# Optimization experiments

Measured on AMD Instinct MI355X. Metric: run time of the kernel, lower is better.

Reference implementation:

```python
import jax, jax.numpy as jnp
import numpy as np

B = 4            # batch (num sequences)
T = 1024         # tokens per sequence (prefill, context_length == tokens_per_seq)
D_MODEL = 4096
H = 32           # n_heads
KVH = 8          # n_kv_heads
HD = D_MODEL // H          # 128
NREP = H // KVH            # 4
BLOCK = 16                 # kv-cache block size
NBLK_PER_SEQ = T // BLOCK  # 64
NBLK = B * NBLK_PER_SEQ    # 256
LAYER_IDX = 0


def _rope(x, positions, cos, sin):
    # x: [N, h, HD]; cos/sin: [max_pos, HD//2]
    c = cos[positions][:, None, :]
    s = sin[positions][:, None, :]
    x1 = x[..., 0::2]
    x2 = x[..., 1::2]
    out = jnp.stack([x1 * c - x2 * s, x1 * s + x2 * c], axis=-1)
    return out.reshape(x.shape)


def setup_inputs() -> dict:
    key = jax.random.key(0)
    ks = jax.random.split(key, 4)
    N = B * T
    x = jax.random.normal(ks[0], (N, D_MODEL), jnp.float32) * 0.02
    w_q = jax.random.normal(ks[1], (D_MODEL, H * HD), jnp.float32) * 0.02
    w_kv = jax.random.normal(ks[2], (D_MODEL, 2 * KVH * HD), jnp.float32) * 0.02
    w_o = jax.random.normal(ks[3], (H * HD, D_MODEL), jnp.float32) * 0.02
    k_cache = jnp.zeros((NBLK, 1, KVH, BLOCK, HD), jnp.float32)
    v_cache = jnp.zeros((NBLK, 1, KVH, BLOCK, HD), jnp.float32)
    # per-token absolute positions: each sequence is a full prefill 0..T-1
    positions = jnp.tile(jnp.arange(T, dtype=jnp.int32), B)          # [N]
    block_tables = jnp.arange(NBLK, dtype=jnp.int32).reshape(B, NBLK_PER_SEQ)
    inv_freq = 1.0 / (10000.0 ** (jnp.arange(0, HD, 2, dtype=jnp.float32) / HD))
    ang = jnp.arange(T, dtype=jnp.float32)[:, None] * inv_freq[None, :]
    rope_cos = jnp.cos(ang)
    rope_sin = jnp.sin(ang)
    return dict(x=x, w_q=w_q, w_kv=w_kv, w_o=w_o, k_cache=k_cache,
                v_cache=v_cache, rope_cos=rope_cos, rope_sin=rope_sin,
                positions=positions, block_tables=block_tables)


def reference(x, w_q, w_kv, w_o, k_cache, v_cache, rope_cos, rope_sin,
              positions, block_tables):
    N = x.shape[0]
    q = (x @ w_q).reshape(N, H, HD)
    k, v = jnp.split(x @ w_kv, 2, axis=-1)
    k = k.reshape(N, KVH, HD)
    v = v.reshape(N, KVH, HD)
    q = _rope(q, positions, rope_cos, rope_sin)
    k = _rope(k, positions, rope_cos, rope_sin)

    # scatter new K/V into the paged cache via block-table indirection
    seq_idx = jnp.repeat(jnp.arange(B), T)                 # [N]
    blk = block_tables[seq_idx, positions // BLOCK]        # [N]
    off = positions % BLOCK                                # [N]
    k_cache = k_cache.at[blk, LAYER_IDX, :, off, :].set(k)
    v_cache = v_cache.at[blk, LAYER_IDX, :, off, :].set(v)

    # gather full context K/V for every sequence from the cache
    kpos = jnp.arange(T, dtype=jnp.int32)
    gblk = block_tables[:, kpos // BLOCK]                  # [B, T]
    goff = (kpos % BLOCK)[None, :]                         # [1, T] -> broadcast
    gk = k_cache[gblk, LAYER_IDX, :, goff, :]              # [B, T, KVH, HD]
    gv = v_cache[gblk, LAYER_IDX, :, goff, :]

    # GQA: repeat kv heads (repeat_interleave over head dim)
    gk = jnp.repeat(gk, NREP, axis=2)                      # [B, T, H, HD]
    gv = jnp.repeat(gv, NREP, axis=2)

    qb = q.reshape(B, T, H, HD)
    scores = jnp.einsum('bqhd,bkhd->bhqk', qb, gk) / jnp.sqrt(jnp.float32(HD))
    qpos = positions.reshape(B, T)
    causal = qpos[:, None, :, None] < kpos[None, None, None, :]  # mask where q < k
    scores = jnp.where(causal, jnp.float32(-1e9), scores)
    probs = jax.nn.softmax(scores.astype(jnp.float32), axis=-1).astype(qb.dtype)
    out = jnp.einsum('bhqk,bkhd->bqhd', probs, gv).reshape(N, H * HD)
    return out @ w_o
```

## Files before the change

kernel.cpp:

```cpp
#include <hip/hip_runtime.h>
#include <hip/hip_bf16.h>


typedef __hip_bfloat16 bf16;
using frag  = __attribute__((ext_vector_type(8))) short;
using facc  = __attribute__((ext_vector_type(4))) float;

static __device__ __forceinline__ bf16 f2b(float x) { return __float2bfloat16(x); }

static __device__ __forceinline__ void async_copy16(const void* g, void* l) {
  __builtin_amdgcn_global_load_lds(
      (const __attribute__((address_space(1))) void*)g,
      (__attribute__((address_space(3))) void*)l, 16, 0, 0);
}

static __device__ __forceinline__ facc mfma16(frag a, frag b, facc c) {
  return __builtin_amdgcn_mfma_f32_16x16x32_bf16(a, b, c, 0, 0, 0);
}

#define SBARRIER() do { __builtin_amdgcn_sched_barrier(0); \
                        __builtin_amdgcn_s_barrier(); \
                        __builtin_amdgcn_sched_barrier(0); } while (0)
#define WAIT_LGKM(n) do { asm volatile("s_waitcnt lgkmcnt(" #n ")" ::: "memory"); \
                          __builtin_amdgcn_sched_barrier(0); } while (0)
#define WAIT_VM(n) do { asm volatile("s_waitcnt vmcnt(" #n ")" ::: "memory"); \
                        __builtin_amdgcn_sched_barrier(0); } while (0)
#define SCHEDBAR() __builtin_amdgcn_sched_barrier(0)
#define PRIO1 __builtin_amdgcn_s_setprio(1)
#define PRIO0 __builtin_amdgcn_s_setprio(0)


__global__ void convert_x_kernel(const float* __restrict__ in, bf16* __restrict__ out) {
  int i = (blockIdx.x * blockDim.x + threadIdx.x) * 4;
  float4 v = *(const float4*)(in + i);
  out[i + 0] = f2b(v.x);
  out[i + 1] = f2b(v.y);
  out[i + 2] = f2b(v.z);
  out[i + 3] = f2b(v.w);
}

__global__ void transpose_conv_kernel(const float* __restrict__ in, bf16* __restrict__ out,
                                      int rows, int cols) {
  __shared__ float tile[32][33];
  int bx = blockIdx.x * 32;
  int by = blockIdx.y * 32;
  int tx = threadIdx.x, ty = threadIdx.y;
#pragma unroll
  for (int i = 0; i < 32; i += 8)
    tile[ty + i][tx] = in[(size_t)(by + ty + i) * cols + bx + tx];
  __syncthreads();
#pragma unroll
  for (int i = 0; i < 32; i += 8)
    out[(size_t)(bx + ty + i) * rows + by + tx] = f2b(tile[tx][ty + i]);
}


template <int KIND>
static __device__ __forceinline__ void stage_half(const bf16* __restrict__ gsrc,
                                                  char* lds, int Kd, int tid) {
#pragma unroll
  for (int i = 0; i < 2; ++i) {
    int c = i * 512 + tid;
    int chunk;
    if (KIND < 2) chunk = c + ((c >> 9) << 9) + (KIND == 1 ? 512 : 0);
    else          chunk = c + ((c >> 8) << 8) + (KIND == 3 ? 256 : 0);
    int r  = chunk >> 3;
    int gc = (chunk & 7) ^ (r & 7);
    async_copy16(gsrc + (size_t)r * Kd + gc * 8, lds + (size_t)chunk * 16);
  }
}

#define RDA(DST, BUF, MH)                                         \
  _Pragma("unroll")                                               \
  for (int mt = 0; mt < 4; ++mt) {                                \
    DST[mt][0] = lda(BUF, MH, mt, 0);                             \
    DST[mt][1] = lda(BUF, MH, mt, 1);                             \
  }

#define RDB(DST, BUF, NH)                                         \
  _Pragma("unroll")                                               \
  for (int nt = 0; nt < 2; ++nt) {                                \
    DST[nt][0] = ldb(BUF, NH, nt, 0);                             \
    DST[nt][1] = ldb(BUF, NH, nt, 1);                             \
  }

#define MFMA_Q(AF, BF, MB, NB)                                    \
  _Pragma("unroll")                                               \
  for (int mt = 0; mt < 4; ++mt)                                  \
    _Pragma("unroll")                                             \
    for (int nt = 0; nt < 2; ++nt) {                              \
      acc[(MB) + mt][(NB) + nt] =                                 \
          mfma16(AF[mt][0], BF[nt][0], acc[(MB) + mt][(NB) + nt]);\
      acc[(MB) + mt][(NB) + nt] =                                 \
          mfma16(AF[mt][1], BF[nt][1], acc[(MB) + mt][(NB) + nt]);\
    }

#define GTILE(AC, BC, AN, BN, B0C, B0N, T)                        \
  {                                                               \
    bool s1 = (T) + 1 < NKT;                                      \
    bool s2 = (T) + 2 < NKT;                                      \
    const bf16* Ag1 = Ag + (size_t)((T) + 1) * 64;                \
    const bf16* Ag2 = Ag + (size_t)((T) + 2) * 64;                \
    const bf16* Bg2 = Bg + (size_t)((T) + 2) * 64;                \
                                 \
    if (s1) stage_half<1>(Ag1, AN, Kd, tid);                      \
    RDB(b1, BC, 1);                                               \
    SBARRIER();                                                   \
    WAIT_LGKM(4);                                                 \
    PRIO1; MFMA_Q(af, B0C, 0, 0); PRIO0;                          \
    WAIT_VM(8);                                                   \
    SBARRIER();                                                   \
                  \
    if (s2) stage_half<2>(Bg2, (char*)(BC), Kd, tid);             \
    SBARRIER();                                                   \
    WAIT_LGKM(0);                                                 \
    PRIO1; MFMA_Q(af, b1, 0, 2); PRIO0;                           \
    SCHEDBAR();                                                   \
    RDA(af, AC, 1);                                               \
    SBARRIER();                                                   \
                                 \
    if (s2) stage_half<0>(Ag2, (char*)(AC), Kd, tid);             \
    SBARRIER();                                                   \
    WAIT_LGKM(0);                                                 \
    PRIO1; MFMA_Q(af, b1, 4, 2); PRIO0;                           \
    WAIT_VM(8);                                                   \
    SBARRIER();                                                   \
    \
    if (s2) stage_half<3>(Bg2, (char*)(BC), Kd, tid);             \
    if (s1) { RDB(B0N, BN, 0); }                                  \
    SBARRIER();                                                   \
    PRIO1; MFMA_Q(af, B0C, 4, 0); PRIO0;                          \
    SCHEDBAR();                                                   \
    if (s1) { RDA(af, AN, 0); }                                   \
    WAIT_VM(8);                                                   \
    SBARRIER();                                                   \
  }

template <bool OUT_F32>
__global__ __launch_bounds__(512, 2) void gemm256_kernel(
    const bf16* __restrict__ A, const bf16* __restrict__ BT,
    void* __restrict__ Cout, int M, int Nn, int Kd) {
  extern __shared__ char smem[];
  char* As0 = smem;
  char* As1 = smem + 32 * 1024;
  char* Bs0 = smem + 64 * 1024;
  char* Bs1 = smem + 96 * 1024;

  int tid  = threadIdx.x;
  int wave = tid >> 6, lane = tid & 63;
  int ml   = lane & 15, quad = lane >> 4;
  int wm   = wave >> 2, wn = wave & 3;

  int nbx = Nn >> 8;
  int nwg = gridDim.x;
  int id  = blockIdx.x;
  int swz = (id & 7) * (nwg >> 3) + (id >> 3);
  int bm  = (swz / nbx) << 8;
  int bn  = (swz % nbx) << 8;

  const bf16* Ag = A + (size_t)bm * Kd;
  const bf16* Bg = BT + (size_t)bn * Kd;

  facc acc[8][4];
#pragma unroll
  for (int i = 0; i < 8; ++i)
#pragma unroll
    for (int j = 0; j < 4; ++j)
#pragma unroll
      for (int r = 0; r < 4; ++r) acc[i][j][r] = 0.f;

  auto lda = [&](const char* buf, int mh, int mt, int kk) -> frag {
    int row = wm * 128 + mh * 64 + mt * 16 + ml;
    int cs  = (kk * 4 + quad) ^ (ml & 7);
    return *(const frag*)(buf + ((size_t)row * 8 + cs) * 16);
  };
  auto ldb = [&](const char* buf, int nh, int nt, int kk) -> frag {
    int row = wn * 64 + nh * 32 + nt * 16 + ml;
    int cs  = (kk * 4 + quad) ^ (ml & 7);
    return *(const frag*)(buf + ((size_t)row * 8 + cs) * 16);
  };

  int NKT = Kd >> 6;

  frag af[4][2], b0e[2][2], b0o[2][2], b1[2][2];

  stage_half<2>(Bg,      Bs0, Kd, tid);
  stage_half<0>(Ag,      As0, Kd, tid);
  stage_half<3>(Bg,      Bs0, Kd, tid);
  stage_half<1>(Ag,      As0, Kd, tid);
  stage_half<2>(Bg + 64, Bs1, Kd, tid);
  stage_half<0>(Ag + 64, As1, Kd, tid);
  stage_half<3>(Bg + 64, Bs1, Kd, tid);
  WAIT_VM(10);
  SBARRIER();
  RDB(b0e, Bs0, 0);
  SCHEDBAR();
  RDA(af, As0, 0);
  WAIT_VM(8);
  SBARRIER();

  for (int kt = 0; kt < NKT; kt += 2) {
    GTILE(As0, Bs0, As1, Bs1, b0e, b0o, kt);
    GTILE(As1, Bs1, As0, Bs0, b0o, b0e, kt + 1);
  }

#pragma unroll
  for (int mi = 0; mi < 8; ++mi)
#pragma unroll
    for (int ni = 0; ni < 4; ++ni)
#pragma unroll
      for (int r = 0; r < 4; ++r) {
        size_t row = bm + wm * 128 + mi * 16 + quad * 4 + r;
        size_t col = bn + wn * 64 + ni * 16 + ml;
        float v = acc[mi][ni][r];
        if (OUT_F32) ((float*)Cout)[row * Nn + col] = v;
        else         ((bf16*)Cout)[row * Nn + col] = f2b(v);
      }
}


template <int KIND>
static __device__ __forceinline__ void stage_kv(const bf16* __restrict__ gsrc,
                                                char* lds, int Kd, int tid) {
  if (KIND < 2) {
#pragma unroll
    for (int i = 0; i < 2; ++i) {
      int c = i * 512 + tid;
      int chunk = c + ((c >> 8) << 8) + (KIND == 1 ? 256 : 0);
      int r  = chunk >> 3;
      int gc = (chunk & 7) ^ (r & 7);
      async_copy16(gsrc + (size_t)r * Kd + gc * 8, lds + (size_t)chunk * 16);
    }
  } else {
    int c = tid;
    int chunk = c + ((c >> 8) << 8) + (KIND == 3 ? 256 : 0);
    int r  = chunk >> 3;
    int gc = (chunk & 7) ^ (r & 7);
    async_copy16(gsrc + (size_t)r * Kd + gc * 8, lds + (size_t)chunk * 16);
  }
}

__global__ __launch_bounds__(512, 2) void gemm_kv_kernel(
    const bf16* __restrict__ A, const bf16* __restrict__ BT,
    bf16* __restrict__ Cout, int M, int Nn, int Kd) {
  extern __shared__ char smem[];
  char* As0 = smem;
  char* As1 = smem + 32 * 1024;
  char* Bs0 = smem + 64 * 1024;
  char* Bs1 = smem + 80 * 1024;

  int tid  = threadIdx.x;
  int wave = tid >> 6, lane = tid & 63;
  int ml   = lane & 15, quad = lane >> 4;
  int wm   = wave >> 1, wn = wave & 1;

  int nbx = Nn >> 7;
  int nwg = gridDim.x;
  int id  = blockIdx.x;
  int swz = (id & 7) * (nwg >> 3) + (id >> 3);
  int bm  = (swz / nbx) << 8;
  int bn  = (swz % nbx) << 7;

  const bf16* Ag = A + (size_t)bm * Kd;
  const bf16* Bg = BT + (size_t)bn * Kd;

  facc acc[4][4];
#pragma unroll
  for (int i = 0; i < 4; ++i)
#pragma unroll
    for (int j = 0; j < 4; ++j)
#pragma unroll
      for (int r = 0; r < 4; ++r) acc[i][j][r] = 0.f;

  auto lda = [&](const char* buf, int mh, int mt, int kk) -> frag {
    int row = wm * 64 + mh * 32 + mt * 16 + ml;
    int cs  = (kk * 4 + quad) ^ (ml & 7);
    return *(const frag*)(buf + ((size_t)row * 8 + cs) * 16);
  };
  auto ldb = [&](const char* buf, int nt, int kk) -> frag {
    int row = wn * 64 + nt * 16 + ml;
    int cs  = (kk * 4 + quad) ^ (ml & 7);
    return *(const frag*)(buf + ((size_t)row * 8 + cs) * 16);
  };

  int NKT = Kd >> 6;

  frag af[2][2], bf[4][2];

  stage_kv<0>(Ag,      As0, Kd, tid);
  stage_kv<2>(Bg,      Bs0, Kd, tid);
  stage_kv<3>(Bg,      Bs0, Kd, tid);
  stage_kv<1>(Ag,      As0, Kd, tid);
  stage_kv<0>(Ag + 64, As1, Kd, tid);
  stage_kv<2>(Bg + 64, Bs1, Kd, tid);
  stage_kv<3>(Bg + 64, Bs1, Kd, tid);
  WAIT_VM(6);
  SBARRIER();

  for (int kt = 0; kt < NKT; ++kt) {
    const char* Ac = (kt & 1) ? As1 : As0;
    const char* Bc = (kt & 1) ? Bs1 : Bs0;
    char* An = (kt & 1) ? As0 : As1;
    bool s1 = kt + 1 < NKT;
    bool s2 = kt + 2 < NKT;
    const bf16* Ag1 = Ag + (size_t)(kt + 1) * 64;
    const bf16* Ag2 = Ag + (size_t)(kt + 2) * 64;
    const bf16* Bg2 = Bg + (size_t)(kt + 2) * 64;

    if (s1) stage_kv<1>(Ag1, An, Kd, tid);
#pragma unroll
    for (int mt = 0; mt < 2; ++mt) {
      af[mt][0] = lda(Ac, 0, mt, 0);
      af[mt][1] = lda(Ac, 0, mt, 1);
    }
#pragma unroll
    for (int nt = 0; nt < 4; ++nt) {
      bf[nt][0] = ldb(Bc, nt, 0);
      bf[nt][1] = ldb(Bc, nt, 1);
    }
    SBARRIER();
    WAIT_LGKM(0);
    PRIO1;
#pragma unroll
    for (int mt = 0; mt < 2; ++mt)
#pragma unroll
      for (int nt = 0; nt < 4; ++nt) {
        acc[mt][nt] = mfma16(af[mt][0], bf[nt][0], acc[mt][nt]);
        acc[mt][nt] = mfma16(af[mt][1], bf[nt][1], acc[mt][nt]);
      }
    PRIO0;
    if (s1) { WAIT_VM(6); } else { WAIT_VM(0); }
    SBARRIER();

    if (s2) {
      stage_kv<0>(Ag2, (char*)Ac, Kd, tid);
      stage_kv<2>(Bg2, (char*)Bc, Kd, tid);
      stage_kv<3>(Bg2, (char*)Bc, Kd, tid);
    }
#pragma unroll
    for (int mt = 0; mt < 2; ++mt) {
      af[mt][0] = lda(Ac, 1, mt, 0);
      af[mt][1] = lda(Ac, 1, mt, 1);
    }
    SBARRIER();
    WAIT_LGKM(0);
    PRIO1;
#pragma unroll
    for (int mt = 0; mt < 2; ++mt)
#pragma unroll
      for (int nt = 0; nt < 4; ++nt) {
        acc[2 + mt][nt] = mfma16(af[mt][0], bf[nt][0], acc[2 + mt][nt]);
        acc[2 + mt][nt] = mfma16(af[mt][1], bf[nt][1], acc[2 + mt][nt]);
      }
    PRIO0;
    if (s1) {
      if (s2) { WAIT_VM(6); } else { WAIT_VM(2); }
      SBARRIER();
    }
  }

#pragma unroll
  for (int mi = 0; mi < 4; ++mi)
#pragma unroll
    for (int ni = 0; ni < 4; ++ni)
#pragma unroll
      for (int r = 0; r < 4; ++r) {
        size_t row = bm + wm * 64 + (mi >> 1) * 32 + (mi & 1) * 16 + quad * 4 + r;
        size_t col = bn + wn * 64 + ni * 16 + ml;
        Cout[row * Nn + col] = f2b(acc[mi][ni][r]);
      }
}


__global__ void rope_kernel(bf16* __restrict__ qh, bf16* __restrict__ kvb,
                            const float* __restrict__ cosb, const float* __restrict__ sinb,
                            const int* __restrict__ positions) {
  const float qscale = 0.08838834764831843f;
  int idx   = blockIdx.x * blockDim.x + threadIdx.x;
  int token = idx / 2560;
  int p     = idx % 2560;
  int pos   = positions[token];
  bf16* base;
  int i;
  float sc;
  if (p < 2048) {
    int hh = p >> 6; i = p & 63;
    base = qh + (size_t)token * 4096 + hh * 128 + 2 * i;
    sc = qscale;
  } else {
    int pk = p - 2048;
    int hh = pk >> 6; i = pk & 63;
    base = kvb + (size_t)token * 2048 + hh * 128 + 2 * i;
    sc = 1.0f;
  }
  float c = cosb[pos * 64 + i] * sc, s = sinb[pos * 64 + i] * sc;
  float x1 = __bfloat162float(base[0]);
  float x2 = __bfloat162float(base[1]);
  base[0] = f2b(x1 * c - x2 * s);
  base[1] = f2b(x1 * s + x2 * c);
}


__global__ void vtrans_kernel(const bf16* __restrict__ kvb, bf16* __restrict__ vt) {
  __shared__ bf16 tile[32][33];
  int dt = blockIdx.x * 32;
  int tt = blockIdx.y * 32;
  int bk = blockIdx.z;
  int b = bk >> 3, kvh = bk & 7;
  const bf16* in = kvb + (size_t)(b * 1024) * 2048 + 1024 + kvh * 128;
  bf16* out = vt + (size_t)bk * 128 * 1024;
  int tx = threadIdx.x, ty = threadIdx.y;
#pragma unroll
  for (int i = 0; i < 32; i += 8)
    tile[ty + i][tx] = in[(size_t)(tt + ty + i) * 2048 + dt + tx];
  __syncthreads();
#pragma unroll
  for (int i = 0; i < 32; i += 8)
    out[(size_t)(dt + ty + i) * 1024 + tt + tx] = tile[tx][ty + i];
}


__global__ __launch_bounds__(512, 4) void attn_kernel(
    const bf16* __restrict__ qh, const bf16* __restrict__ kvb,
    const bf16* __restrict__ vt, bf16* __restrict__ attn) {
  __shared__ alignas(16) bf16 Ks[64 * 128];
  __shared__ alignas(16) bf16 Vs[128 * 64];
  __shared__ alignas(16) bf16 Ps[8][16 * 84];

  int tid  = threadIdx.x;
  int wave = tid >> 6;
  int lane = tid & 63;
  int ml   = lane & 15, quad = lane >> 4;
  int wq   = wave >> 2;
  int wh   = wave & 3;

  int pr  = blockIdx.x;
  int kvh = blockIdx.y;
  int b   = blockIdx.z;
  int h   = kvh * 4 + wh;

  const bf16* kbptr = kvb + (size_t)(b * 1024) * 2048 + kvh * 128;
  const bf16* vbptr = vt + (size_t)((b * 8 + kvh) * 128) * 1024;
  bf16* Pw = &Ps[wave][0];

#pragma unroll
  for (int half = 0; half < 2; ++half) {
    int qtile = half ? pr : (31 - pr);
    int q0 = qtile * 32 + wq * 16;

    frag qf[4];
    const bf16* qrow = qh + (size_t)(b * 1024 + q0 + ml) * 4096 + h * 128;
#pragma unroll
    for (int s = 0; s < 4; ++s) qf[s] = *(const frag*)(qrow + s * 32 + quad * 8);

    facc o[8];
#pragma unroll
    for (int db = 0; db < 8; ++db)
#pragma unroll
      for (int r = 0; r < 4; ++r) o[db][r] = 0.f;
    float m_i[4], l_i[4];
#pragma unroll
    for (int r = 0; r < 4; ++r) { m_i[r] = -1e30f; l_i[r] = 0.f; }

    int nkb = (qtile >> 1) + 1;

    for (int kb = 0; kb < nkb; ++kb) {
      int kbase = kb * 64;
      __syncthreads();
#pragma unroll
      for (int i = 0; i < 2; ++i) {
        int c = i * 512 + tid;
        int row = c >> 4, cs = c & 15;
        int gc = cs ^ (row & 7);
        async_copy16(kbptr + (size_t)(kbase + row) * 2048 + gc * 8, (char*)Ks + c * 16);
      }
#pragma unroll
      for (int i = 0; i < 2; ++i) {
        int c = i * 512 + tid;
        int d = c >> 3, cs = c & 7;
        int gc = cs ^ (d & 7);
        async_copy16(vbptr + (size_t)d * 1024 + kbase + gc * 8, (char*)Vs + c * 16);
      }
      __syncthreads();

      facc sc[4];
#pragma unroll
      for (int kt = 0; kt < 4; ++kt)
#pragma unroll
        for (int r = 0; r < 4; ++r) sc[kt][r] = 0.f;
#pragma unroll
      for (int s = 0; s < 4; ++s)
#pragma unroll
        for (int kt = 0; kt < 4; ++kt) {
          int row = kt * 16 + ml;
          int cs = ((s * 4 + quad) ^ (ml & 7));
          frag kf = *(const frag*)&Ks[row * 128 + cs * 8];
          sc[kt] = __builtin_amdgcn_mfma_f32_16x16x32_bf16(qf[s], kf, sc[kt], 0, 0, 0);
        }

#pragma unroll
      for (int r = 0; r < 4; ++r) {
        int qp = q0 + quad * 4 + r;
        float v[4];
        float mx = -1e30f;
#pragma unroll
        for (int kt = 0; kt < 4; ++kt) {
          float s = sc[kt][r];
          if (qp < kbase + kt * 16 + ml) s = -1e30f;
          v[kt] = s;
          mx = fmaxf(mx, s);
        }
        mx = fmaxf(mx, __shfl_xor(mx, 1));
        mx = fmaxf(mx, __shfl_xor(mx, 2));
        mx = fmaxf(mx, __shfl_xor(mx, 4));
        mx = fmaxf(mx, __shfl_xor(mx, 8));
        float mnew  = fmaxf(m_i[r], mx);
        float alpha = __expf(m_i[r] - mnew);
        m_i[r] = mnew;
        float ps = 0.f;
#pragma unroll
        for (int kt = 0; kt < 4; ++kt) {
          float p = __expf(v[kt] - mnew);
          ps += p;
          Pw[(quad * 4 + r) * 84 + kt * 16 + ml] = f2b(p);
        }
        ps += __shfl_xor(ps, 1);
        ps += __shfl_xor(ps, 2);
        ps += __shfl_xor(ps, 4);
        ps += __shfl_xor(ps, 8);
        l_i[r] = l_i[r] * alpha + ps;
#pragma unroll
        for (int db = 0; db < 8; ++db) o[db][r] *= alpha;
      }
      __syncthreads();

#pragma unroll
      for (int j = 0; j < 2; ++j) {
        frag pf = *(const frag*)&Pw[ml * 84 + j * 32 + quad * 8];
#pragma unroll
        for (int db = 0; db < 8; ++db) {
          int d = db * 16 + ml;
          int cs = ((j * 4 + quad) ^ (ml & 7));
          frag vf = *(const frag*)&Vs[d * 64 + cs * 8];
          o[db] = __builtin_amdgcn_mfma_f32_16x16x32_bf16(pf, vf, o[db], 0, 0, 0);
        }
      }
    }

    bf16* arow = attn + (size_t)(b * 1024 + q0) * 4096 + h * 128;
#pragma unroll
    for (int db = 0; db < 8; ++db)
#pragma unroll
      for (int r = 0; r < 4; ++r) {
        float v = o[db][r] / l_i[r];
        arow[(size_t)(quad * 4 + r) * 4096 + db * 16 + ml] = f2b(v);
      }
  }
}


extern "C" void kernel_launch(void* const* d_in, const int* in_sizes, int n_in,
                              void* d_out, int out_size, void* d_ws, size_t ws_size,
                              hipStream_t stream) {
  const float* x        = (const float*)d_in[0];
  const float* w_q      = (const float*)d_in[1];
  const float* w_kv     = (const float*)d_in[2];
  const float* w_o      = (const float*)d_in[3];
  const float* rope_cos = (const float*)d_in[6];
  const float* rope_sin = (const float*)d_in[7];
  const int*   positions = (const int*)d_in[8];
  float* out = (float*)d_out;

  char* ws = (char*)d_ws;
  const size_t MB = 1024 * 1024;
  bf16* xb    = (bf16*)(ws + 0);
  bf16* wqT   = (bf16*)(ws + 32 * MB);
  bf16* wkvT  = (bf16*)(ws + 64 * MB);
  bf16* woT   = (bf16*)(ws + 80 * MB);
  bf16* qh    = (bf16*)(ws + 112 * MB);
  bf16* kvb   = (bf16*)(ws + 144 * MB);
  bf16* vt    = (bf16*)(ws + 160 * MB);
  bf16* attnb = xb;

  static bool s_attr = false;
  if (!s_attr) {
    hipFuncSetAttribute(reinterpret_cast<const void*>(gemm256_kernel<false>),
                        hipFuncAttributeMaxDynamicSharedMemorySize, 131072);
    hipFuncSetAttribute(reinterpret_cast<const void*>(gemm256_kernel<true>),
                        hipFuncAttributeMaxDynamicSharedMemorySize, 131072);
    hipFuncSetAttribute(reinterpret_cast<const void*>(gemm_kv_kernel),
                        hipFuncAttributeMaxDynamicSharedMemorySize, 98304);
    s_attr = true;
  }

  convert_x_kernel<<<16384, 256, 0, stream>>>(x, xb);
  transpose_conv_kernel<<<dim3(128, 128), dim3(32, 8), 0, stream>>>(w_q, wqT, 4096, 4096);
  transpose_conv_kernel<<<dim3(64, 128),  dim3(32, 8), 0, stream>>>(w_kv, wkvT, 4096, 2048);
  transpose_conv_kernel<<<dim3(128, 128), dim3(32, 8), 0, stream>>>(w_o, woT, 4096, 4096);

  gemm256_kernel<false><<<dim3(256), 512, 131072, stream>>>(xb, wqT, qh, 4096, 4096, 4096);
  gemm_kv_kernel<<<dim3(256), 512, 98304, stream>>>(xb, wkvT, kvb, 4096, 2048, 4096);

  rope_kernel<<<40960, 256, 0, stream>>>(qh, kvb, rope_cos, rope_sin, positions);
  vtrans_kernel<<<dim3(4, 32, 32), dim3(32, 8), 0, stream>>>(kvb, vt);

  attn_kernel<<<dim3(16, 8, 4), 512, 0, stream>>>(qh, kvb, vt, attnb);

  gemm256_kernel<true><<<dim3(256), 512, 131072, stream>>>(attnb, woT, out, 4096, 4096, 4096);
}
```

Measured before the change: 685.8 us.

## Double-buffer A fragments and prefetch B half earlier in GEMM pipeline

New measurement: 1.057 ms. 1.54x slower.

```diff
diff --git a/kernel.cpp b/kernel.cpp
--- a/kernel.cpp
+++ b/kernel.cpp
@@ -102,37 +102,37 @@
     const bf16* Ag1 = Ag + (size_t)((T) + 1) * 64;                \
     const bf16* Ag2 = Ag + (size_t)((T) + 2) * 64;                \
     const bf16* Bg2 = Bg + (size_t)((T) + 2) * 64;                \
+    \
+    if (s1) stage_half<1>(Ag1, AN, Kd, tid);                      \
+    RDA(af1, AC, 1);                                              \
+    SBARRIER();                                                   \
+    WAIT_LGKM(12);                                                \
+    PRIO1; MFMA_Q(af0, B0C, 0, 0); PRIO0;                         \
+    SBARRIER();                                                   \
                                  \
-    if (s1) stage_half<1>(Ag1, AN, Kd, tid);                      \
-    RDB(b1, BC, 1);                                               \
-    SBARRIER();                                                   \
-    WAIT_LGKM(4);                                                 \
-    PRIO1; MFMA_Q(af, B0C, 0, 0); PRIO0;                          \
-    WAIT_VM(8);                                                   \
-    SBARRIER();                                                   \
-                  \
     if (s2) stage_half<2>(Bg2, (char*)(BC), Kd, tid);             \
     SBARRIER();                                                   \
-    WAIT_LGKM(0);                                                 \
-    PRIO1; MFMA_Q(af, b1, 0, 2); PRIO0;                           \
-    SCHEDBAR();                                                   \
-    RDA(af, AC, 1);                                               \
-    SBARRIER();                                                   \
-                                 \
+    WAIT_LGKM(8);                                                 \
+    PRIO1; MFMA_Q(af0, b1, 0, 2); PRIO0;                          \
+    if (s2)      { WAIT_VM(6); }                                  \
+    else if (s1) { WAIT_VM(4); }                                  \
+    SBARRIER();                                                   \
+       \
     if (s2) stage_half<0>(Ag2, (char*)(AC), Kd, tid);             \
-    SBARRIER();                                                   \
-    WAIT_LGKM(0);                                                 \
-    PRIO1; MFMA_Q(af, b1, 4, 2); PRIO0;                           \
-    WAIT_VM(8);                                                   \
-    SBARRIER();                                                   \
-    \
+    if (s1) { RDA(af0, AN, 0); }                                  \
+    SBARRIER();                                                   \
+    if (s1) { WAIT_LGKM(8); } else { WAIT_LGKM(0); }              \
+    PRIO1; MFMA_Q(af1, b1, 4, 2); PRIO0;                          \
+    if (s2)      { WAIT_VM(6); }                                  \
+    else if (s1) { WAIT_VM(2); }                                  \
+    SBARRIER();                                                   \
+      \
     if (s2) stage_half<3>(Bg2, (char*)(BC), Kd, tid);             \
-    if (s1) { RDB(B0N, BN, 0); }                                  \
-    SBARRIER();                                                   \
-    PRIO1; MFMA_Q(af, B0C, 4, 0); PRIO0;                          \
-    SCHEDBAR();                                                   \
-    if (s1) { RDA(af, AN, 0); }                                   \
-    WAIT_VM(8);                                                   \
+    if (s1) { RDB(B0N, BN, 0); RDB(b1, BN, 1); }                  \
+    SBARRIER();                                                   \
+    PRIO1; MFMA_Q(af1, B0C, 4, 0); PRIO0;                         \
+    if (s2)      { WAIT_VM(6); }                                  \
+    else if (s1) { WAIT_VM(0); }                                  \
     SBARRIER();                                                   \
   }
 
@@ -182,7 +182,7 @@
 
   int NKT = Kd >> 6;
 
-  frag af[4][2], b0e[2][2], b0o[2][2], b1[2][2];
+  frag af0[4][2], af1[4][2], b0e[2][2], b0o[2][2], b1[2][2];
 
   stage_half<2>(Bg,      Bs0, Kd, tid);
   stage_half<0>(Ag,      As0, Kd, tid);
@@ -191,12 +191,12 @@
   stage_half<2>(Bg + 64, Bs1, Kd, tid);
   stage_half<0>(Ag + 64, As1, Kd, tid);
   stage_half<3>(Bg + 64, Bs1, Kd, tid);
-  WAIT_VM(10);
+  WAIT_VM(8);
   SBARRIER();
+  RDA(af0, As0, 0);
   RDB(b0e, Bs0, 0);
-  SCHEDBAR();
-  RDA(af, As0, 0);
-  WAIT_VM(8);
+  RDB(b1,  Bs0, 1);
+  WAIT_VM(6);
   SBARRIER();
 
   for (int kt = 0; kt < NKT; kt += 2) {
```
